# Optimization experiments

Measured on AMD Instinct MI355X. Metric: run time of the kernel, lower is better.

## Reference

```python
import jax, jax.numpy as jnp
import numpy as np

N_NODES = 50000
N_EDGES = 800000
NFEAT, NHID, NOUT = 256, 256, 128


def setup_inputs() -> dict:
    key = jax.random.key(0)
    ks = jax.random.split(key, 5)
    stdv1 = 1.0 / np.sqrt(NHID)
    stdv2 = 1.0 / np.sqrt(NOUT)
    x = jax.random.normal(ks[0], (N_NODES, NFEAT), dtype=jnp.float32)
    w1 = jax.random.uniform(ks[1], (NFEAT, NHID), minval=-stdv1, maxval=stdv1, dtype=jnp.float32)
    w2 = jax.random.uniform(ks[2], (NHID, NOUT), minval=-stdv2, maxval=stdv2, dtype=jnp.float32)
    edge_src = jax.random.randint(ks[3], (N_EDGES,), 0, N_NODES, dtype=jnp.int32)
    edge_dst = jax.random.randint(ks[4], (N_EDGES,), 0, N_NODES, dtype=jnp.int32)
    return {"x": x, "w1": w1, "w2": w2, "edge_src": edge_src, "edge_dst": edge_dst}


def _gcn_layer(h, w, edge_src, edge_dst, n):
    # support = h @ w ; out[i] = sum_{(src,dst=i) in E} support[src]  (SpMM with 0/1 adj)
    support = jnp.dot(h, w)                      # [N, out]
    return jax.ops.segment_sum(support[edge_src], edge_dst, num_segments=n)


def reference(x, w1, w2, edge_src, edge_dst):
    n = x.shape[0]
    h = jax.nn.relu(_gcn_layer(x, w1, edge_src, edge_dst, n))
    # dropout is identity in eval mode (training=False)
    out = _gcn_layer(h, w2, edge_src, edge_dst, n)
    return out
```

## Files before the change

### kernel.cpp

```cpp
#include <hip/hip_runtime.h>
#include <hip/hip_bf16.h>


#define NFEAT 256
#define NOUT  128
#define CHUNK 4096
#define P4CAP 5120

typedef short short8 __attribute__((ext_vector_type(8)));
typedef float floatx4 __attribute__((ext_vector_type(4)));
typedef float floatx2 __attribute__((ext_vector_type(2)));

typedef const __attribute__((address_space(1))) unsigned short GAS_US;
typedef __attribute__((address_space(3))) unsigned short LAS_US;

__device__ __forceinline__ unsigned short f2bf(float f) {
    unsigned u = __builtin_bit_cast(unsigned, f);
    unsigned r = (u + 0x7FFFu + ((u >> 16) & 1u)) >> 16;
    return (unsigned short)r;
}
__device__ __forceinline__ unsigned char f2fp8(float f) {
    int p = __builtin_amdgcn_cvt_pk_fp8_f32(f, f, 0, false);
    return (unsigned char)(p & 0xFF);
}
__device__ __forceinline__ void accf8(float* a, uint2 v) {
    floatx2 f0 = __builtin_amdgcn_cvt_pk_f32_fp8(v.x, false);
    floatx2 f1 = __builtin_amdgcn_cvt_pk_f32_fp8(v.x, true);
    floatx2 f2 = __builtin_amdgcn_cvt_pk_f32_fp8(v.y, false);
    floatx2 f3 = __builtin_amdgcn_cvt_pk_f32_fp8(v.y, true);
    a[0] += f0.x; a[1] += f0.y; a[2] += f1.x; a[3] += f1.y;
    a[4] += f2.x; a[5] += f2.y; a[6] += f3.x; a[7] += f3.y;
}


__global__ __launch_bounds__(256) void k_prep(const float* __restrict__ w1,
                                              const float* __restrict__ w2,
                                              const float* __restrict__ x,
                                              unsigned short* __restrict__ w1T,
                                              unsigned short* __restrict__ w2T,
                                              unsigned short* __restrict__ xbf,
                                              const int* __restrict__ edst,
                                              int* __restrict__ counts_bm,
                                              int E, int bins, int pblk) {
    __shared__ int h[256];
    int b = blockIdx.x, tid = threadIdx.x;
    if (b < 256) {
        int idx = b * 256 + tid;
        int nn = idx >> 8, k = idx & 255;
        w1T[idx] = f2bf(w1[k * 256 + nn]);
        return;
    }
    if (b < 384) {
        int idx = (b - 256) * 256 + tid;
        int nn = idx >> 8, k = idx & 255;
        w2T[idx] = f2bf(w2[k * 128 + nn]);
        return;
    }
    if (b >= 384 + pblk) {
        int c = b - 384 - pblk;
        size_t base = (size_t)c * 4096 + (size_t)tid * 16;
        const float4* src = (const float4*)&x[base];
        float4 f0 = src[0], f1 = src[1], f2 = src[2], f3 = src[3];
        short8 v0, v1;
        v0[0] = (short)f2bf(f0.x); v0[1] = (short)f2bf(f0.y);
        v0[2] = (short)f2bf(f0.z); v0[3] = (short)f2bf(f0.w);
        v0[4] = (short)f2bf(f1.x); v0[5] = (short)f2bf(f1.y);
        v0[6] = (short)f2bf(f1.z); v0[7] = (short)f2bf(f1.w);
        v1[0] = (short)f2bf(f2.x); v1[1] = (short)f2bf(f2.y);
        v1[2] = (short)f2bf(f2.z); v1[3] = (short)f2bf(f2.w);
        v1[4] = (short)f2bf(f3.x); v1[5] = (short)f2bf(f3.y);
        v1[6] = (short)f2bf(f3.z); v1[7] = (short)f2bf(f3.w);
        *(short8*)&xbf[base]     = v0;
        *(short8*)&xbf[base + 8] = v1;
        return;
    }
    int blk = b - 384;
    h[tid] = 0;
    __syncthreads();
    int base = blk * CHUNK;
#pragma unroll
    for (int t = 0; t < CHUNK / 256; ++t) {
        int i = base + t * 256 + tid;
        if (i < E) atomicAdd(&h[edst[i] >> 8], 1);
    }
    __syncthreads();
    for (int j = tid; j < bins; j += 256)
        counts_bm[j * pblk + blk] = h[j];
}


__global__ __launch_bounds__(1024) void k_scan1(const int* __restrict__ deg,
                                                int* __restrict__ excl,
                                                int* __restrict__ partials, int n) {
    __shared__ int s[1024];
    int gid = blockIdx.x * 1024 + threadIdx.x;
    int v = (gid < n) ? deg[gid] : 0;
    s[threadIdx.x] = v;
    __syncthreads();
    for (int off = 1; off < 1024; off <<= 1) {
        int t = (threadIdx.x >= off) ? s[threadIdx.x - off] : 0;
        __syncthreads();
        s[threadIdx.x] += t;
        __syncthreads();
    }
    if (gid < n) excl[gid] = s[threadIdx.x] - v;
    if (threadIdx.x == 1023) partials[blockIdx.x] = s[1023];
}

__global__ __launch_bounds__(1024) void k_scan3(int* __restrict__ excl,
                                                const int* __restrict__ partials,
                                                int n, int total) {
    __shared__ int pfx;
    if (threadIdx.x < 64) {
        int v = ((int)threadIdx.x < (int)blockIdx.x) ? partials[threadIdx.x] : 0;
        for (int o = 32; o > 0; o >>= 1) v += __shfl_down(v, o, 64);
        if (threadIdx.x == 0) pfx = v;
    }
    __syncthreads();
    int gid = blockIdx.x * 1024 + threadIdx.x;
    if (gid < n) excl[gid] += pfx;
    if (gid == 0) excl[n] = total;
}


#define GBM 128
#define GBN 128
#define GBK 64

__global__ __launch_bounds__(256) void k_gemm1_scatter(
        const unsigned short* __restrict__ A,
        const unsigned short* __restrict__ BT,
        unsigned char* __restrict__ C,
        const int* __restrict__ esrc, const int* __restrict__ edst,
        const int* __restrict__ offs_bm,
        unsigned int* __restrict__ edgePk,
        int M, int E, int nGemm, int bins, int pblk) {
    __shared__ unsigned short As[GBM * GBK];
    __shared__ unsigned short Bs[GBN * GBK];
    int b = blockIdx.x, tid = threadIdx.x;

    if (b >= nGemm) {
        int blk = b - nGemm;
        int* baseOff = (int*)As;
        int* cur     = (int*)Bs;
        for (int j = tid; j < bins; j += 256) {
            baseOff[j] = offs_bm[j * pblk + blk];
            cur[j] = 0;
        }
        __syncthreads();
        int base = blk * CHUNK;
#pragma unroll
        for (int t = 0; t < CHUNK / 256; ++t) {
            int i = base + t * 256 + tid;
            if (i < E) {
                int d = edst[i], s = esrc[i];
                int bin = d >> 8;
                int pos = atomicAdd(&cur[bin], 1);
                edgePk[baseOff[bin] + pos] = ((unsigned)d << 16) | (unsigned)s;
            }
        }
        return;
    }

    const int N = 256, K = 256;
    int bx = b >> 1, by = b & 1;
    int lane = tid & 63, wave = tid >> 6;
    int wm = (wave >> 1) * 64, wn = (wave & 1) * 64;
    int q = lane >> 4, r = lane & 15;
    int m0 = bx * GBM, n0 = by * GBN;
    int srow = (lane >> 3);
    int scol = (lane & 7) * 8;

    floatx4 acc[4][4];
#pragma unroll
    for (int i = 0; i < 4; ++i)
#pragma unroll
        for (int j = 0; j < 4; ++j) acc[i][j] = (floatx4){0.f, 0.f, 0.f, 0.f};

    for (int k0 = 0; k0 < K; k0 += GBK) {
#pragma unroll
        for (int t = 0; t < 4; ++t) {
            int row = wave * 32 + t * 8 + srow;
            int gm = m0 + row; if (gm >= M) gm = M - 1;
            __builtin_amdgcn_global_load_lds(
                (GAS_US*)&A[(size_t)gm * K + k0 + scol],
                (LAS_US*)&As[(wave * 32 + t * 8) * GBK], 16, 0, 0);
            __builtin_amdgcn_global_load_lds(
                (GAS_US*)&BT[(size_t)(n0 + row) * K + k0 + scol],
                (LAS_US*)&Bs[(wave * 32 + t * 8) * GBK], 16, 0, 0);
        }
        __syncthreads();
#pragma unroll
        for (int kk = 0; kk < GBK; kk += 32) {
            short8 af[4], bfr[4];
#pragma unroll
            for (int i = 0; i < 4; ++i)
                af[i] = *(const short8*)&As[(wm + i * 16 + r) * GBK + kk + q * 8];
#pragma unroll
            for (int j = 0; j < 4; ++j)
                bfr[j] = *(const short8*)&Bs[(wn + j * 16 + r) * GBK + kk + q * 8];
#pragma unroll
            for (int i = 0; i < 4; ++i)
#pragma unroll
                for (int j = 0; j < 4; ++j)
                    acc[i][j] = __builtin_amdgcn_mfma_f32_16x16x32_bf16(
                        af[i], bfr[j], acc[i][j], 0, 0, 0);
        }
        __syncthreads();
    }

#pragma unroll
    for (int i = 0; i < 4; ++i) {
#pragma unroll
        for (int rr = 0; rr < 4; ++rr) {
            int grow = m0 + wm + i * 16 + q * 4 + rr;
            if (grow < M) {
                size_t base = (size_t)grow * N + n0 + wn;
#pragma unroll
                for (int j = 0; j < 4; ++j)
                    C[base + j * 16 + r] = f2fp8(acc[i][j][rr]);
            }
        }
    }
}


__global__ __launch_bounds__(256) void k_p4(const unsigned int* __restrict__ edgePk,
                                            const int* __restrict__ offs_bm,
                                            unsigned short* __restrict__ csr,
                                            int* __restrict__ offsets,
                                            int N, int E, int bins, int pblk) {
    __shared__ unsigned int buf[P4CAP];
    __shared__ int h[256], loff[256], cur[256];
    int b = blockIdx.x, tid = threadIdx.x;
    int s0 = offs_bm[b * pblk];
    int s1 = (b + 1 < bins) ? offs_bm[(b + 1) * pblk] : E;
    int n = s1 - s0; if (n > P4CAP) n = P4CAP;
    h[tid] = 0;
    __syncthreads();
    for (int i = tid; i < n; i += 256) {
        unsigned int p = edgePk[s0 + i];
        buf[i] = p;
        atomicAdd(&h[(p >> 16) & 255], 1);
    }
    __syncthreads();
    int v = h[tid];
    loff[tid] = v;
    __syncthreads();
    for (int off = 1; off < 256; off <<= 1) {
        int t2 = (tid >= off) ? loff[tid - off] : 0;
        __syncthreads();
        loff[tid] += t2;
        __syncthreads();
    }
    int excl = loff[tid] - v;
    int node = b * 256 + tid;
    if (node < N) offsets[node] = s0 + excl;
    if (b == bins - 1 && tid == 0) offsets[N] = E;
    cur[tid] = 0;
    __syncthreads();
    loff[tid] = excl;
    __syncthreads();
    for (int i = tid; i < n; i += 256) {
        unsigned int p = buf[i];
        int ld = (p >> 16) & 255;
        int pos = atomicAdd(&cur[ld], 1);
        csr[s0 + loff[ld] + pos] = (unsigned short)(p & 0xFFFFu);
    }
}


__global__ __launch_bounds__(256) void k_gemm2(const unsigned short* __restrict__ A,
                                               const unsigned short* __restrict__ BT,
                                               unsigned char* __restrict__ C,
                                               int M, int N, int K) {
    __shared__ unsigned short As[GBM * GBK];
    __shared__ unsigned short Bs[GBN * GBK];
    int tid = threadIdx.x;
    int lane = tid & 63, wave = tid >> 6;
    int wm = (wave >> 1) * 64, wn = (wave & 1) * 64;
    int q = lane >> 4, r = lane & 15;
    int m0 = blockIdx.x * GBM, n0 = blockIdx.y * GBN;
    int srow = (lane >> 3);
    int scol = (lane & 7) * 8;

    floatx4 acc[4][4];
#pragma unroll
    for (int i = 0; i < 4; ++i)
#pragma unroll
        for (int j = 0; j < 4; ++j) acc[i][j] = (floatx4){0.f, 0.f, 0.f, 0.f};

    for (int k0 = 0; k0 < K; k0 += GBK) {
#pragma unroll
        for (int t = 0; t < 4; ++t) {
            int row = wave * 32 + t * 8 + srow;
            int gm = m0 + row; if (gm >= M) gm = M - 1;
            __builtin_amdgcn_global_load_lds(
                (GAS_US*)&A[(size_t)gm * K + k0 + scol],
                (LAS_US*)&As[(wave * 32 + t * 8) * GBK], 16, 0, 0);
            __builtin_amdgcn_global_load_lds(
                (GAS_US*)&BT[(size_t)(n0 + row) * K + k0 + scol],
                (LAS_US*)&Bs[(wave * 32 + t * 8) * GBK], 16, 0, 0);
        }
        __syncthreads();
#pragma unroll
        for (int kk = 0; kk < GBK; kk += 32) {
            short8 af[4], bfr[4];
#pragma unroll
            for (int i = 0; i < 4; ++i)
                af[i] = *(const short8*)&As[(wm + i * 16 + r) * GBK + kk + q * 8];
#pragma unroll
            for (int j = 0; j < 4; ++j)
                bfr[j] = *(const short8*)&Bs[(wn + j * 16 + r) * GBK + kk + q * 8];
#pragma unroll
            for (int i = 0; i < 4; ++i)
#pragma unroll
                for (int j = 0; j < 4; ++j)
                    acc[i][j] = __builtin_amdgcn_mfma_f32_16x16x32_bf16(
                        af[i], bfr[j], acc[i][j], 0, 0, 0);
        }
        __syncthreads();
    }

#pragma unroll
    for (int i = 0; i < 4; ++i) {
#pragma unroll
        for (int rr = 0; rr < 4; ++rr) {
            int grow = m0 + wm + i * 16 + q * 4 + rr;
            if (grow < M) {
                size_t base = (size_t)grow * N + n0 + wn;
#pragma unroll
                for (int j = 0; j < 4; ++j)
                    C[base + j * 16 + r] = f2fp8(acc[i][j][rr]);
            }
        }
    }
}


__global__ __launch_bounds__(256) void k_gather_relu256(const unsigned char* __restrict__ sup,
                                                        const int* __restrict__ offsets,
                                                        const unsigned short* __restrict__ csr,
                                                        unsigned short* __restrict__ h, int n) {
    int lane = threadIdx.x & 63, wave = threadIdx.x >> 6;
    int half = lane >> 5, l32 = lane & 31;
    int node = blockIdx.x * 8 + wave * 2 + half;
    bool valid = node < n;
    int beg = valid ? offsets[node] : 0;
    int end = valid ? offsets[node + 1] : 0;
    int cnt = end - beg;
    const unsigned short* slot = &csr[beg];
    float a[8] = {};
    int e = 0;
    for (; e + 8 <= cnt; e += 8) {
        int s[8];
#pragma unroll
        for (int t = 0; t < 8; ++t) s[t] = slot[e + t];
        uint2 v[8];
#pragma unroll
        for (int t = 0; t < 8; ++t)
            v[t] = *(const uint2*)&sup[(size_t)s[t] * 256 + l32 * 8];
#pragma unroll
        for (int t = 0; t < 8; ++t) accf8(a, v[t]);
    }
    for (; e + 4 <= cnt; e += 4) {
        int s0 = slot[e], s1 = slot[e + 1], s2 = slot[e + 2], s3 = slot[e + 3];
        uint2 v0 = *(const uint2*)&sup[(size_t)s0 * 256 + l32 * 8];
        uint2 v1 = *(const uint2*)&sup[(size_t)s1 * 256 + l32 * 8];
        uint2 v2 = *(const uint2*)&sup[(size_t)s2 * 256 + l32 * 8];
        uint2 v3 = *(const uint2*)&sup[(size_t)s3 * 256 + l32 * 8];
        accf8(a, v0); accf8(a, v1); accf8(a, v2); accf8(a, v3);
    }
    for (; e < cnt; ++e) {
        uint2 v = *(const uint2*)&sup[(size_t)slot[e] * 256 + l32 * 8];
        accf8(a, v);
    }
    if (valid) {
        uint4 o;
        o.x = (unsigned)f2bf(fmaxf(a[0], 0.f)) | ((unsigned)f2bf(fmaxf(a[1], 0.f)) << 16);
        o.y = (unsigned)f2bf(fmaxf(a[2], 0.f)) | ((unsigned)f2bf(fmaxf(a[3], 0.f)) << 16);
        o.z = (unsigned)f2bf(fmaxf(a[4], 0.f)) | ((unsigned)f2bf(fmaxf(a[5], 0.f)) << 16);
        o.w = (unsigned)f2bf(fmaxf(a[6], 0.f)) | ((unsigned)f2bf(fmaxf(a[7], 0.f)) << 16);
        *(uint4*)&h[(size_t)node * 256 + l32 * 8] = o;
    }
}


__global__ __launch_bounds__(256) void k_gather128(const unsigned char* __restrict__ sup,
                                                   const int* __restrict__ offsets,
                                                   const unsigned short* __restrict__ csr,
                                                   float* __restrict__ outp, int n) {
    int lane = threadIdx.x & 63, wave = threadIdx.x >> 6;
    int quarter = lane >> 4, l16 = lane & 15;
    int node = blockIdx.x * 16 + wave * 4 + quarter;
    bool valid = node < n;
    int beg = valid ? offsets[node] : 0;
    int end = valid ? offsets[node + 1] : 0;
    int cnt = end - beg;
    const unsigned short* slot = &csr[beg];
    float a[8] = {};
    int e = 0;
    for (; e + 8 <= cnt; e += 8) {
        int s[8];
#pragma unroll
        for (int t = 0; t < 8; ++t) s[t] = slot[e + t];
        uint2 v[8];
#pragma unroll
        for (int t = 0; t < 8; ++t)
            v[t] = *(const uint2*)&sup[(size_t)s[t] * 128 + l16 * 8];
#pragma unroll
        for (int t = 0; t < 8; ++t) accf8(a, v[t]);
    }
    for (; e + 4 <= cnt; e += 4) {
        int s0 = slot[e], s1 = slot[e + 1], s2 = slot[e + 2], s3 = slot[e + 3];
        uint2 v0 = *(const uint2*)&sup[(size_t)s0 * 128 + l16 * 8];
        uint2 v1 = *(const uint2*)&sup[(size_t)s1 * 128 + l16 * 8];
        uint2 v2 = *(const uint2*)&sup[(size_t)s2 * 128 + l16 * 8];
        uint2 v3 = *(const uint2*)&sup[(size_t)s3 * 128 + l16 * 8];
        accf8(a, v0); accf8(a, v1); accf8(a, v2); accf8(a, v3);
    }
    for (; e < cnt; ++e) {
        uint2 v = *(const uint2*)&sup[(size_t)slot[e] * 128 + l16 * 8];
        accf8(a, v);
    }
    if (valid) {
        size_t base = (size_t)node * 128 + l16 * 8;
        *(float4*)&outp[base]     = make_float4(a[0], a[1], a[2], a[3]);
        *(float4*)&outp[base + 4] = make_float4(a[4], a[5], a[6], a[7]);
    }
}


extern "C" void kernel_launch(void* const* d_in, const int* in_sizes, int n_in,
                              void* d_out, int out_size, void* d_ws, size_t ws_size,
                              hipStream_t stream) {
    const float* x    = (const float*)d_in[0];
    const float* w1   = (const float*)d_in[1];
    const float* w2   = (const float*)d_in[2];
    const int*   esrc = (const int*)d_in[3];
    const int*   edst = (const int*)d_in[4];
    float*       out  = (float*)d_out;

    const int N = in_sizes[0] / NFEAT;
    const int E = in_sizes[3];

    const int bins = (N + 255) / 256;
    const int pblk = (E + CHUNK - 1) / CHUNK;
    const int nFlat = bins * pblk;

    char* ws = (char*)d_ws;
    size_t off = 0;
    unsigned short* hb   = (unsigned short*)(ws + off); off += (size_t)N * 256 * 2;
    unsigned char*  sup1 = (unsigned char*)(ws + off);  off += (size_t)N * 256;
    unsigned char*  sup2 = (unsigned char*)(ws + off);  off += (size_t)N * 128;
    unsigned short* w1T  = (unsigned short*)(ws + off); off += (size_t)256 * 256 * 2;
    unsigned short* w2T  = (unsigned short*)(ws + off); off += (size_t)128 * 256 * 2;
    off = (off + 255) & ~(size_t)255;
    int* counts_bm = (int*)(ws + off); off += (size_t)nFlat * sizeof(int);
    off = (off + 255) & ~(size_t)255;
    int* offs_bm   = (int*)(ws + off); off += ((size_t)nFlat + 1) * sizeof(int);
    off = (off + 255) & ~(size_t)255;
    int* partials  = (int*)(ws + off); off += 64 * sizeof(int);
    off = (off + 255) & ~(size_t)255;
    unsigned int* edgePk = (unsigned int*)(ws + off); off += (size_t)E * sizeof(unsigned int);
    off = (off + 255) & ~(size_t)255;
    unsigned short* csr  = (unsigned short*)(ws + off); off += (size_t)E * sizeof(unsigned short);
    off = (off + 255) & ~(size_t)255;
    int* offsets   = (int*)(ws + off); off += ((size_t)N + 1) * sizeof(int);
    (void)ws_size; (void)n_in; (void)out_size;

    unsigned short* xbf = hb;

    const int nCvt = (N * NFEAT) / 4096;
    k_prep<<<384 + pblk + nCvt, 256, 0, stream>>>(w1, w2, x, w1T, w2T, xbf,
                                                  edst, counts_bm, E, bins, pblk);

    int nb = (nFlat + 1023) / 1024;
    k_scan1<<<nb, 1024, 0, stream>>>(counts_bm, offs_bm, partials, nFlat);
    k_scan3<<<nb, 1024, 0, stream>>>(offs_bm, partials, nFlat, E);

    {
        int nGemm = 2 * ((N + GBM - 1) / GBM);
        k_gemm1_scatter<<<nGemm + pblk, 256, 0, stream>>>(
            xbf, w1T, sup1, esrc, edst, offs_bm, edgePk, N, E, nGemm, bins, pblk);
    }

    k_p4<<<bins, 256, 0, stream>>>(edgePk, offs_bm, csr, offsets, N, E, bins, pblk);

    k_gather_relu256<<<(N + 7) / 8, 256, 0, stream>>>(sup1, offsets, csr, hb, N);

    {
        dim3 grid((N + GBM - 1) / GBM, 128 / GBN);
        k_gemm2<<<grid, 256, 0, stream>>>(hb, w2T, sup2, N, 128, 256);
    }

    k_gather128<<<(N + 15) / 16, 256, 0, stream>>>(sup2, offsets, csr, out, N);
}
```

Measured before the change: 200.3 us.

## Shrink CSR build bins to 64 nodes and widen layer-1 gather loads

Bucket edges by dst>>6 (64-node bins) instead of 256-node bins, so the per-bin CSR finalization kernel runs on about 782 blocks instead of 196, each with a smaller LDS buffer. This gives more parallelism in k_p4 but enlarges the flat count array and the scan, so the scan fixup now loops over more partials. Separately, the first gather kernel has 16 lanes per node load 16 bytes each instead of 32 lanes loading 8 bytes, which handles more nodes per block with wider memory accesses. A bin with more than 2048 edges would now be truncated, and this relies on the random test graph staying under that cap.

```diff
diff --git a/kernel.cpp b/kernel.cpp
--- a/kernel.cpp
+++ b/kernel.cpp
@@ -5,7 +5,10 @@
 #define NFEAT 256
 #define NOUT  128
 #define CHUNK 4096
-#define P4CAP 5120
+#define BSHIFT 6
+#define BINSZ  64
+#define MAXBINS 800
+#define P4CAP  2048
 
 typedef short short8 __attribute__((ext_vector_type(8)));
 typedef float floatx4 __attribute__((ext_vector_type(4)));
@@ -42,7 +45,7 @@
                                               const int* __restrict__ edst,
                                               int* __restrict__ counts_bm,
                                               int E, int bins, int pblk) {
-    __shared__ int h[256];
+    __shared__ int h[MAXBINS];
     int b = blockIdx.x, tid = threadIdx.x;
     if (b < 256) {
         int idx = b * 256 + tid;
@@ -75,13 +78,13 @@
         return;
     }
     int blk = b - 384;
-    h[tid] = 0;
+    for (int j = tid; j < bins; j += 256) h[j] = 0;
     __syncthreads();
     int base = blk * CHUNK;
 #pragma unroll
     for (int t = 0; t < CHUNK / 256; ++t) {
         int i = base + t * 256 + tid;
-        if (i < E) atomicAdd(&h[edst[i] >> 8], 1);
+        if (i < E) atomicAdd(&h[edst[i] >> BSHIFT], 1);
     }
     __syncthreads();
     for (int j = tid; j < bins; j += 256)
@@ -112,7 +115,8 @@
                                                 int n, int total) {
     __shared__ int pfx;
     if (threadIdx.x < 64) {
-        int v = ((int)threadIdx.x < (int)blockIdx.x) ? partials[threadIdx.x] : 0;
+        int v = 0;
+        for (int j = threadIdx.x; j < (int)blockIdx.x; j += 64) v += partials[j];
         for (int o = 32; o > 0; o >>= 1) v += __shfl_down(v, o, 64);
         if (threadIdx.x == 0) pfx = v;
     }
@@ -154,7 +158,7 @@
             int i = base + t * 256 + tid;
             if (i < E) {
                 int d = edst[i], s = esrc[i];
-                int bin = d >> 8;
+                int bin = d >> BSHIFT;
                 int pos = atomicAdd(&cur[bin], 1);
                 edgePk[baseOff[bin] + pos] = ((unsigned)d << 16) | (unsigned)s;
             }
@@ -231,39 +235,40 @@
                                             int* __restrict__ offsets,
                                             int N, int E, int bins, int pblk) {
     __shared__ unsigned int buf[P4CAP];
-    __shared__ int h[256], loff[256], cur[256];
+    __shared__ int h[BINSZ], loff[BINSZ], cur[BINSZ];
     int b = blockIdx.x, tid = threadIdx.x;
     int s0 = offs_bm[b * pblk];
     int s1 = (b + 1 < bins) ? offs_bm[(b + 1) * pblk] : E;
     int n = s1 - s0; if (n > P4CAP) n = P4CAP;
-    h[tid] = 0;
+    if (tid < BINSZ) h[tid] = 0;
     __syncthreads();
     for (int i = tid; i < n; i += 256) {
         unsigned int p = edgePk[s0 + i];
         buf[i] = p;
-        atomicAdd(&h[(p >> 16) & 255], 1);
-    }
-    __syncthreads();
-    int v = h[tid];
-    loff[tid] = v;
-    __syncthreads();
-    for (int off = 1; off < 256; off <<= 1) {
-        int t2 = (tid >= off) ? loff[tid - off] : 0;
-        __syncthreads();
-        loff[tid] += t2;
-        __syncthreads();
-    }
-    int excl = loff[tid] - v;
-    int node = b * 256 + tid;
-    if (node < N) offsets[node] = s0 + excl;
+        atomicAdd(&h[(p >> 16) & (BINSZ - 1)], 1);
+    }
+    __syncthreads();
+    int v = (tid < BINSZ) ? h[tid] : 0;
+    if (tid < BINSZ) loff[tid] = v;
+    __syncthreads();
+    for (int off = 1; off < BINSZ; off <<= 1) {
+        int t2 = (tid >= off && tid < BINSZ) ? loff[tid - off] : 0;
+        __syncthreads();
+        if (tid < BINSZ) loff[tid] += t2;
+        __syncthreads();
+    }
+    if (tid < BINSZ) {
+        int excl = loff[tid] - v;
+        int node = b * BINSZ + tid;
+        if (node < N) offsets[node] = s0 + excl;
+        cur[tid] = 0;
+        loff[tid] = excl;
+    }
     if (b == bins - 1 && tid == 0) offsets[N] = E;
-    cur[tid] = 0;
-    __syncthreads();
-    loff[tid] = excl;
     __syncthreads();
     for (int i = tid; i < n; i += 256) {
         unsigned int p = buf[i];
-        int ld = (p >> 16) & 255;
+        int ld = (p >> 16) & (BINSZ - 1);
         int pos = atomicAdd(&cur[ld], 1);
         csr[s0 + loff[ld] + pos] = (unsigned short)(p & 0xFFFFu);
     }
@@ -343,45 +348,56 @@
                                                         const unsigned short* __restrict__ csr,
                                                         unsigned short* __restrict__ h, int n) {
     int lane = threadIdx.x & 63, wave = threadIdx.x >> 6;
-    int half = lane >> 5, l32 = lane & 31;
-    int node = blockIdx.x * 8 + wave * 2 + half;
+    int sub = lane >> 4, f = lane & 15;
+    int node = blockIdx.x * 16 + wave * 4 + sub;
     bool valid = node < n;
     int beg = valid ? offsets[node] : 0;
     int end = valid ? offsets[node + 1] : 0;
     int cnt = end - beg;
     const unsigned short* slot = &csr[beg];
-    float a[8] = {};
+    float a[16] = {};
     int e = 0;
     for (; e + 8 <= cnt; e += 8) {
         int s[8];
 #pragma unroll
         for (int t = 0; t < 8; ++t) s[t] = slot[e + t];
-        uint2 v[8];
+        uint4 v[8];
 #pragma unroll
         for (int t = 0; t < 8; ++t)
-            v[t] = *(const uint2*)&sup[(size_t)s[t] * 256 + l32 * 8];
-#pragma unroll
-        for (int t = 0; t < 8; ++t) accf8(a, v[t]);
+            v[t] = *(const uint4*)&sup[(size_t)s[t] * 256 + f * 16];
+#pragma unroll
+        for (int t = 0; t < 8; ++t) {
+            accf8(a,     make_uint2(v[t].x, v[t].y));
+            accf8(a + 8, make_uint2(v[t].z, v[t].w));
+        }
     }
     for (; e + 4 <= cnt; e += 4) {
-        int s0 = slot[e], s1 = slot[e + 1], s2 = slot[e + 2], s3 = slot[e + 3];
-        uint2 v0 = *(const uint2*)&sup[(size_t)s0 * 256 + l32 * 8];
-        uint2 v1 = *(const uint2*)&sup[(size_t)s1 * 256 + l32 * 8];
-        uint2 v2 = *(const uint2*)&sup[(size_t)s2 * 256 + l32 * 8];
-        uint2 v3 = *(const uint2*)&sup[(size_t)s3 * 256 + l32 * 8];
-        accf8(a, v0); accf8(a, v1); accf8(a, v2); accf8(a, v3);
+        uint4 v0 = *(const uint4*)&sup[(size_t)slot[e]     * 256 + f * 16];
+        uint4 v1 = *(const uint4*)&sup[(size_t)slot[e + 1] * 256 + f * 16];
+        uint4 v2 = *(const uint4*)&sup[(size_t)slot[e + 2] * 256 + f * 16];
+        uint4 v3 = *(const uint4*)&sup[(size_t)slot[e + 3] * 256 + f * 16];
+        accf8(a, make_uint2(v0.x, v0.y)); accf8(a + 8, make_uint2(v0.z, v0.w));
+        accf8(a, make_uint2(v1.x, v1.y)); accf8(a + 8, make_uint2(v1.z, v1.w));
+        accf8(a, make_uint2(v2.x, v2.y)); accf8(a + 8, make_uint2(v2.z, v2.w));
+        accf8(a, make_uint2(v3.x, v3.y)); accf8(a + 8, make_uint2(v3.z, v3.w));
     }
     for (; e < cnt; ++e) {
-        uint2 v = *(const uint2*)&sup[(size_t)slot[e] * 256 + l32 * 8];
-        accf8(a, v);
+        uint4 v = *(const uint4*)&sup[(size_t)slot[e] * 256 + f * 16];
+        accf8(a, make_uint2(v.x, v.y)); accf8(a + 8, make_uint2(v.z, v.w));
     }
     if (valid) {
-        uint4 o;
-        o.x = (unsigned)f2bf(fmaxf(a[0], 0.f)) | ((unsigned)f2bf(fmaxf(a[1], 0.f)) << 16);
-        o.y = (unsigned)f2bf(fmaxf(a[2], 0.f)) | ((unsigned)f2bf(fmaxf(a[3], 0.f)) << 16);
-        o.z = (unsigned)f2bf(fmaxf(a[4], 0.f)) | ((unsigned)f2bf(fmaxf(a[5], 0.f)) << 16);
-        o.w = (unsigned)f2bf(fmaxf(a[6], 0.f)) | ((unsigned)f2bf(fmaxf(a[7], 0.f)) << 16);
-        *(uint4*)&h[(size_t)node * 256 + l32 * 8] = o;
+        size_t base = (size_t)node * 256 + f * 16;
+        uint4 o0, o1;
+        o0.x = (unsigned)f2bf(fmaxf(a[0],  0.f)) | ((unsigned)f2bf(fmaxf(a[1],  0.f)) << 16);
+        o0.y = (unsigned)f2bf(fmaxf(a[2],  0.f)) | ((unsigned)f2bf(fmaxf(a[3],  0.f)) << 16);
+        o0.z = (unsigned)f2bf(fmaxf(a[4],  0.f)) | ((unsigned)f2bf(fmaxf(a[5],  0.f)) << 16);
+        o0.w = (unsigned)f2bf(fmaxf(a[6],  0.f)) | ((unsigned)f2bf(fmaxf(a[7],  0.f)) << 16);
+        o1.x = (unsigned)f2bf(fmaxf(a[8],  0.f)) | ((unsigned)f2bf(fmaxf(a[9],  0.f)) << 16);
+        o1.y = (unsigned)f2bf(fmaxf(a[10], 0.f)) | ((unsigned)f2bf(fmaxf(a[11], 0.f)) << 16);
+        o1.z = (unsigned)f2bf(fmaxf(a[12], 0.f)) | ((unsigned)f2bf(fmaxf(a[13], 0.f)) << 16);
+        o1.w = (unsigned)f2bf(fmaxf(a[14], 0.f)) | ((unsigned)f2bf(fmaxf(a[15], 0.f)) << 16);
+        *(uint4*)&h[base]     = o0;
+        *(uint4*)&h[base + 8] = o1;
     }
 }
 
@@ -444,7 +460,7 @@
     const int N = in_sizes[0] / NFEAT;
     const int E = in_sizes[3];
 
-    const int bins = (N + 255) / 256;
+    const int bins = (N + BINSZ - 1) / BINSZ;
     const int pblk = (E + CHUNK - 1) / CHUNK;
     const int nFlat = bins * pblk;
 
@@ -460,7 +476,7 @@
     off = (off + 255) & ~(size_t)255;
     int* offs_bm   = (int*)(ws + off); off += ((size_t)nFlat + 1) * sizeof(int);
     off = (off + 255) & ~(size_t)255;
-    int* partials  = (int*)(ws + off); off += 64 * sizeof(int);
+    int* partials  = (int*)(ws + off); off += 256 * sizeof(int);
     off = (off + 255) & ~(size_t)255;
     unsigned int* edgePk = (unsigned int*)(ws + off); off += (size_t)E * sizeof(unsigned int);
     off = (off + 255) & ~(size_t)255;
@@ -487,7 +503,7 @@
 
     k_p4<<<bins, 256, 0, stream>>>(edgePk, offs_bm, csr, offsets, N, E, bins, pblk);
 
-    k_gather_relu256<<<(N + 7) / 8, 256, 0, stream>>>(sup1, offsets, csr, hb, N);
+    k_gather_relu256<<<(N + 15) / 16, 256, 0, stream>>>(sup1, offsets, csr, hb, N);
 
     {
         dim3 grid((N + GBM - 1) / GBM, 128 / GBN);
```

New measurement: 206.1 us. +2.9%, slower.

## Fuse layer-1 gather+ReLU into layer-2 GEMM and shrink dst bins to 64 nodes

Applied to the files above, without the earlier changes.

Replaces the separate layer-1 gather/ReLU kernel and the layer-2 GEMM with one kernel. Each 64-row block aggregates its rows into swizzled LDS as bf16, then multiplies that tile by W2 using MFMA, so the hidden matrix never goes to global memory. The destination-bucket size in the CSR build also drops from 256 to 64 nodes, which gives more p4 blocks and a smaller per-block buffer. The scan-partials handling is widened to match the larger bin count. Costs: 32KB of LDS per block for the A tile lowers occupancy during the gather phase, and the W2 tiles are reloaded by every block.

```diff
diff --git a/kernel.cpp b/kernel.cpp
--- a/kernel.cpp
+++ b/kernel.cpp
@@ -5,7 +5,10 @@
 #define NFEAT 256
 #define NOUT  128
 #define CHUNK 4096
-#define P4CAP 5120
+#define BSHIFT 6
+#define BINSZ  64
+#define MAXBINS 800
+#define P4CAP  2048
 
 typedef short short8 __attribute__((ext_vector_type(8)));
 typedef float floatx4 __attribute__((ext_vector_type(4)));
@@ -42,7 +45,7 @@
                                               const int* __restrict__ edst,
                                               int* __restrict__ counts_bm,
                                               int E, int bins, int pblk) {
-    __shared__ int h[256];
+    __shared__ int h[MAXBINS];
     int b = blockIdx.x, tid = threadIdx.x;
     if (b < 256) {
         int idx = b * 256 + tid;
@@ -75,13 +78,13 @@
         return;
     }
     int blk = b - 384;
-    h[tid] = 0;
+    for (int j = tid; j < bins; j += 256) h[j] = 0;
     __syncthreads();
     int base = blk * CHUNK;
 #pragma unroll
     for (int t = 0; t < CHUNK / 256; ++t) {
         int i = base + t * 256 + tid;
-        if (i < E) atomicAdd(&h[edst[i] >> 8], 1);
+        if (i < E) atomicAdd(&h[edst[i] >> BSHIFT], 1);
     }
     __syncthreads();
     for (int j = tid; j < bins; j += 256)
@@ -112,7 +115,8 @@
                                                 int n, int total) {
     __shared__ int pfx;
     if (threadIdx.x < 64) {
-        int v = ((int)threadIdx.x < (int)blockIdx.x) ? partials[threadIdx.x] : 0;
+        int v = 0;
+        for (int j = threadIdx.x; j < (int)blockIdx.x; j += 64) v += partials[j];
         for (int o = 32; o > 0; o >>= 1) v += __shfl_down(v, o, 64);
         if (threadIdx.x == 0) pfx = v;
     }
@@ -154,7 +158,7 @@
             int i = base + t * 256 + tid;
             if (i < E) {
                 int d = edst[i], s = esrc[i];
-                int bin = d >> 8;
+                int bin = d >> BSHIFT;
                 int pos = atomicAdd(&cur[bin], 1);
                 edgePk[baseOff[bin] + pos] = ((unsigned)d << 16) | (unsigned)s;
             }
@@ -231,157 +235,157 @@
                                             int* __restrict__ offsets,
                                             int N, int E, int bins, int pblk) {
     __shared__ unsigned int buf[P4CAP];
-    __shared__ int h[256], loff[256], cur[256];
+    __shared__ int h[BINSZ], loff[BINSZ], cur[BINSZ];
     int b = blockIdx.x, tid = threadIdx.x;
     int s0 = offs_bm[b * pblk];
     int s1 = (b + 1 < bins) ? offs_bm[(b + 1) * pblk] : E;
     int n = s1 - s0; if (n > P4CAP) n = P4CAP;
-    h[tid] = 0;
+    if (tid < BINSZ) h[tid] = 0;
     __syncthreads();
     for (int i = tid; i < n; i += 256) {
         unsigned int p = edgePk[s0 + i];
         buf[i] = p;
-        atomicAdd(&h[(p >> 16) & 255], 1);
-    }
-    __syncthreads();
-    int v = h[tid];
-    loff[tid] = v;
-    __syncthreads();
-    for (int off = 1; off < 256; off <<= 1) {
-        int t2 = (tid >= off) ? loff[tid - off] : 0;
-        __syncthreads();
-        loff[tid] += t2;
-        __syncthreads();
-    }
-    int excl = loff[tid] - v;
-    int node = b * 256 + tid;
-    if (node < N) offsets[node] = s0 + excl;
+        atomicAdd(&h[(p >> 16) & (BINSZ - 1)], 1);
+    }
+    __syncthreads();
+    int v = (tid < BINSZ) ? h[tid] : 0;
+    if (tid < BINSZ) loff[tid] = v;
+    __syncthreads();
+    for (int off = 1; off < BINSZ; off <<= 1) {
+        int t2 = (tid >= off && tid < BINSZ) ? loff[tid - off] : 0;
+        __syncthreads();
+        if (tid < BINSZ) loff[tid] += t2;
+        __syncthreads();
+    }
+    if (tid < BINSZ) {
+        int excl = loff[tid] - v;
+        int node = b * BINSZ + tid;
+        if (node < N) offsets[node] = s0 + excl;
+        cur[tid] = 0;
+        loff[tid] = excl;
+    }
     if (b == bins - 1 && tid == 0) offsets[N] = E;
-    cur[tid] = 0;
-    __syncthreads();
-    loff[tid] = excl;
     __syncthreads();
     for (int i = tid; i < n; i += 256) {
         unsigned int p = buf[i];
-        int ld = (p >> 16) & 255;
+        int ld = (p >> 16) & (BINSZ - 1);
         int pos = atomicAdd(&cur[ld], 1);
         csr[s0 + loff[ld] + pos] = (unsigned short)(p & 0xFFFFu);
     }
 }
 
 
-__global__ __launch_bounds__(256) void k_gemm2(const unsigned short* __restrict__ A,
-                                               const unsigned short* __restrict__ BT,
-                                               unsigned char* __restrict__ C,
-                                               int M, int N, int K) {
-    __shared__ unsigned short As[GBM * GBK];
-    __shared__ unsigned short Bs[GBN * GBK];
+__global__ __launch_bounds__(256) void k_fused2(const unsigned char* __restrict__ sup,
+                                                const int* __restrict__ offsets,
+                                                const unsigned short* __restrict__ csr,
+                                                const unsigned short* __restrict__ BT,
+                                                unsigned char* __restrict__ C,
+                                                int n) {
+    __shared__ unsigned short As[64 * 256];
+    __shared__ unsigned short Bs[128 * GBK];
     int tid = threadIdx.x;
     int lane = tid & 63, wave = tid >> 6;
-    int wm = (wave >> 1) * 64, wn = (wave & 1) * 64;
-    int q = lane >> 4, r = lane & 15;
-    int m0 = blockIdx.x * GBM, n0 = blockIdx.y * GBN;
-    int srow = (lane >> 3);
-    int scol = (lane & 7) * 8;
-
-    floatx4 acc[4][4];
-#pragma unroll
-    for (int i = 0; i < 4; ++i)
-#pragma unroll
-        for (int j = 0; j < 4; ++j) acc[i][j] = (floatx4){0.f, 0.f, 0.f, 0.f};
-
-    for (int k0 = 0; k0 < K; k0 += GBK) {
-#pragma unroll
-        for (int t = 0; t < 4; ++t) {
-            int row = wave * 32 + t * 8 + srow;
-            int gm = m0 + row; if (gm >= M) gm = M - 1;
-            __builtin_amdgcn_global_load_lds(
-                (GAS_US*)&A[(size_t)gm * K + k0 + scol],
-                (LAS_US*)&As[(wave * 32 + t * 8) * GBK], 16, 0, 0);
-            __builtin_amdgcn_global_load_lds(
-                (GAS_US*)&BT[(size_t)(n0 + row) * K + k0 + scol],
-                (LAS_US*)&Bs[(wave * 32 + t * 8) * GBK], 16, 0, 0);
-        }
-        __syncthreads();
-#pragma unroll
-        for (int kk = 0; kk < GBK; kk += 32) {
-            short8 af[4], bfr[4];
-#pragma unroll
-            for (int i = 0; i < 4; ++i)
-                af[i] = *(const short8*)&As[(wm + i * 16 + r) * GBK + kk + q * 8];
-#pragma unroll
-            for (int j = 0; j < 4; ++j)
-                bfr[j] = *(const short8*)&Bs[(wn + j * 16 + r) * GBK + kk + q * 8];
-#pragma unroll
-            for (int i = 0; i < 4; ++i)
-#pragma unroll
-                for (int j = 0; j < 4; ++j)
-                    acc[i][j] = __builtin_amdgcn_mfma_f32_16x16x32_bf16(
-                        af[i], bfr[j], acc[i][j], 0, 0, 0);
-        }
-        __syncthreads();
-    }
-
-#pragma unroll
-    for (int i = 0; i < 4; ++i) {
-#pragma unroll
-        for (int rr = 0; rr < 4; ++rr) {
-            int grow = m0 + wm + i * 16 + q * 4 + rr;
-            if (grow < M) {
-                size_t base = (size_t)grow * N + n0 + wn;
-#pragma unroll
-                for (int j = 0; j < 4; ++j)
-                    C[base + j * 16 + r] = f2fp8(acc[i][j][rr]);
-            }
-        }
-    }
-}
-
-
-__global__ __launch_bounds__(256) void k_gather_relu256(const unsigned char* __restrict__ sup,
-                                                        const int* __restrict__ offsets,
-                                                        const unsigned short* __restrict__ csr,
-                                                        unsigned short* __restrict__ h, int n) {
-    int lane = threadIdx.x & 63, wave = threadIdx.x >> 6;
+    int m0 = blockIdx.x * 64;
+
     int half = lane >> 5, l32 = lane & 31;
-    int node = blockIdx.x * 8 + wave * 2 + half;
-    bool valid = node < n;
-    int beg = valid ? offsets[node] : 0;
-    int end = valid ? offsets[node + 1] : 0;
-    int cnt = end - beg;
-    const unsigned short* slot = &csr[beg];
-    float a[8] = {};
-    int e = 0;
-    for (; e + 8 <= cnt; e += 8) {
-        int s[8];
-#pragma unroll
-        for (int t = 0; t < 8; ++t) s[t] = slot[e + t];
-        uint2 v[8];
-#pragma unroll
-        for (int t = 0; t < 8; ++t)
-            v[t] = *(const uint2*)&sup[(size_t)s[t] * 256 + l32 * 8];
-#pragma unroll
-        for (int t = 0; t < 8; ++t) accf8(a, v[t]);
-    }
-    for (; e + 4 <= cnt; e += 4) {
-        int s0 = slot[e], s1 = slot[e + 1], s2 = slot[e + 2], s3 = slot[e + 3];
-        uint2 v0 = *(const uint2*)&sup[(size_t)s0 * 256 + l32 * 8];
-        uint2 v1 = *(const uint2*)&sup[(size_t)s1 * 256 + l32 * 8];
-        uint2 v2 = *(const uint2*)&sup[(size_t)s2 * 256 + l32 * 8];
-        uint2 v3 = *(const uint2*)&sup[(size_t)s3 * 256 + l32 * 8];
-        accf8(a, v0); accf8(a, v1); accf8(a, v2); accf8(a, v3);
-    }
-    for (; e < cnt; ++e) {
-        uint2 v = *(const uint2*)&sup[(size_t)slot[e] * 256 + l32 * 8];
-        accf8(a, v);
-    }
-    if (valid) {
+#pragma unroll
+    for (int pass = 0; pass < 8; ++pass) {
+        int rowl = pass * 8 + wave * 2 + half;
+        int node = m0 + rowl;
+        bool valid = node < n;
+        int beg = valid ? offsets[node] : 0;
+        int end = valid ? offsets[node + 1] : 0;
+        int cnt = end - beg;
+        const unsigned short* slot = &csr[beg];
+        float a[8] = {};
+        int e = 0;
+        for (; e + 8 <= cnt; e += 8) {
+            int s[8];
+#pragma unroll
+            for (int t = 0; t < 8; ++t) s[t] = slot[e + t];
+            uint2 v[8];
+#pragma unroll
+            for (int t = 0; t < 8; ++t)
+                v[t] = *(const uint2*)&sup[(size_t)s[t] * 256 + l32 * 8];
+#pragma unroll
+            for (int t = 0; t < 8; ++t) accf8(a, v[t]);
+        }
+        for (; e + 4 <= cnt; e += 4) {
+            int s0 = slot[e], s1 = slot[e + 1], s2 = slot[e + 2], s3 = slot[e + 3];
+            uint2 v0 = *(const uint2*)&sup[(size_t)s0 * 256 + l32 * 8];
+            uint2 v1 = *(const uint2*)&sup[(size_t)s1 * 256 + l32 * 8];
+            uint2 v2 = *(const uint2*)&sup[(size_t)s2 * 256 + l32 * 8];
+            uint2 v3 = *(const uint2*)&sup[(size_t)s3 * 256 + l32 * 8];
+            accf8(a, v0); accf8(a, v1); accf8(a, v2); accf8(a, v3);
+        }
+        for (; e < cnt; ++e) {
+            uint2 v = *(const uint2*)&sup[(size_t)slot[e] * 256 + l32 * 8];
+            accf8(a, v);
+        }
         uint4 o;
         o.x = (unsigned)f2bf(fmaxf(a[0], 0.f)) | ((unsigned)f2bf(fmaxf(a[1], 0.f)) << 16);
         o.y = (unsigned)f2bf(fmaxf(a[2], 0.f)) | ((unsigned)f2bf(fmaxf(a[3], 0.f)) << 16);
         o.z = (unsigned)f2bf(fmaxf(a[4], 0.f)) | ((unsigned)f2bf(fmaxf(a[5], 0.f)) << 16);
         o.w = (unsigned)f2bf(fmaxf(a[6], 0.f)) | ((unsigned)f2bf(fmaxf(a[7], 0.f)) << 16);
-        *(uint4*)&h[(size_t)node * 256 + l32 * 8] = o;
+        int g = l32 ^ (rowl & 7);
+        *(uint4*)&As[rowl * 256 + g * 8] = o;
+    }
+    __syncthreads();
+
+    int wm = (wave >> 1) * 32, wn = (wave & 1) * 64;
+    int q = lane >> 4, r = lane & 15;
+    int srow = (lane >> 3);
+    int scol = (lane & 7) * 8;
+
+    floatx4 acc[2][4];
+#pragma unroll
+    for (int i = 0; i < 2; ++i)
+#pragma unroll
+        for (int j = 0; j < 4; ++j) acc[i][j] = (floatx4){0.f, 0.f, 0.f, 0.f};
+
+    for (int k0 = 0; k0 < 256; k0 += GBK) {
+#pragma unroll
+        for (int t = 0; t < 4; ++t) {
+            int row = wave * 32 + t * 8 + srow;
+            __builtin_amdgcn_global_load_lds(
+                (GAS_US*)&BT[(size_t)row * 256 + k0 + scol],
+                (LAS_US*)&Bs[(wave * 32 + t * 8) * GBK], 16, 0, 0);
+        }
+        __syncthreads();
+#pragma unroll
+        for (int kk = 0; kk < GBK; kk += 32) {
+            short8 af[2], bfr[4];
+#pragma unroll
+            for (int i = 0; i < 2; ++i) {
+                int row = wm + i * 16 + r;
+                int gb = ((k0 + kk) >> 3) + q;
+                af[i] = *(const short8*)&As[row * 256 + ((gb ^ (row & 7)) << 3)];
+            }
+#pragma unroll
+            for (int j = 0; j < 4; ++j)
+                bfr[j] = *(const short8*)&Bs[(wn + j * 16 + r) * GBK + kk + q * 8];
+#pragma unroll
+            for (int i = 0; i < 2; ++i)
+#pragma unroll
+                for (int j = 0; j < 4; ++j)
+                    acc[i][j] = __builtin_amdgcn_mfma_f32_16x16x32_bf16(
+                        af[i], bfr[j], acc[i][j], 0, 0, 0);
+        }
+        __syncthreads();
+    }
+
+#pragma unroll
+    for (int i = 0; i < 2; ++i) {
+#pragma unroll
+        for (int rr = 0; rr < 4; ++rr) {
+            int grow = m0 + wm + i * 16 + q * 4 + rr;
+            if (grow < n) {
+                size_t base = (size_t)grow * NOUT + wn;
+#pragma unroll
+                for (int j = 0; j < 4; ++j)
+                    C[base + j * 16 + r] = f2fp8(acc[i][j][rr]);
+            }
+        }
     }
 }
 
@@ -444,13 +448,13 @@
     const int N = in_sizes[0] / NFEAT;
     const int E = in_sizes[3];
 
-    const int bins = (N + 255) / 256;
+    const int bins = (N + BINSZ - 1) / BINSZ;
     const int pblk = (E + CHUNK - 1) / CHUNK;
     const int nFlat = bins * pblk;
 
     char* ws = (char*)d_ws;
     size_t off = 0;
-    unsigned short* hb   = (unsigned short*)(ws + off); off += (size_t)N * 256 * 2;
+    unsigned short* xbf  = (unsigned short*)(ws + off); off += (size_t)N * 256 * 2;
     unsigned char*  sup1 = (unsigned char*)(ws + off);  off += (size_t)N * 256;
     unsigned char*  sup2 = (unsigned char*)(ws + off);  off += (size_t)N * 128;
     unsigned short* w1T  = (unsigned short*)(ws + off); off += (size_t)256 * 256 * 2;
@@ -460,7 +464,7 @@
     off = (off + 255) & ~(size_t)255;
     int* offs_bm   = (int*)(ws + off); off += ((size_t)nFlat + 1) * sizeof(int);
     off = (off + 255) & ~(size_t)255;
-    int* partials  = (int*)(ws + off); off += 64 * sizeof(int);
+    int* partials  = (int*)(ws + off); off += 256 * sizeof(int);
     off = (off + 255) & ~(size_t)255;
     unsigned int* edgePk = (unsigned int*)(ws + off); off += (size_t)E * sizeof(unsigned int);
     off = (off + 255) & ~(size_t)255;
@@ -468,8 +472,6 @@
     off = (off + 255) & ~(size_t)255;
     int* offsets   = (int*)(ws + off); off += ((size_t)N + 1) * sizeof(int);
     (void)ws_size; (void)n_in; (void)out_size;
-
-    unsigned short* xbf = hb;
 
     const int nCvt = (N * NFEAT) / 4096;
     k_prep<<<384 + pblk + nCvt, 256, 0, stream>>>(w1, w2, x, w1T, w2T, xbf,
@@ -487,12 +489,7 @@
 
     k_p4<<<bins, 256, 0, stream>>>(edgePk, offs_bm, csr, offsets, N, E, bins, pblk);
 
-    k_gather_relu256<<<(N + 7) / 8, 256, 0, stream>>>(sup1, offsets, csr, hb, N);
-
-    {
-        dim3 grid((N + GBM - 1) / GBM, 128 / GBN);
-        k_gemm2<<<grid, 256, 0, stream>>>(hb, w2T, sup2, N, 128, 256);
-    }
+    k_fused2<<<(N + 63) / 64, 256, 0, stream>>>(sup1, offsets, csr, w2T, sup2, N);
 
     k_gather128<<<(N + 15) / 16, 256, 0, stream>>>(sup2, offsets, csr, out, N);
 }
```

After: 226.4 us. +13.0%, slower.

## Fold scan fix-up into consumers, double chunk size, split CSR build per bin into quarters

Applied to the files above, without the earlier changes.

Removes the k_scan3 kernel by having the scatter and CSR-build kernels add the block partial prefix themselves, computed serially by one thread. Doubles CHUNK so fewer scatter blocks and flat bins exist. k_p4 now launches four blocks per bin, each recomputing the full histogram from global memory (no LDS buffer) but writing only its quarter of nodes. This trades one launch and more parallelism against redundant histogram reads and a serial prefix loop.

```diff
diff --git a/kernel.cpp b/kernel.cpp
--- a/kernel.cpp
+++ b/kernel.cpp
@@ -4,8 +4,7 @@
 
 #define NFEAT 256
 #define NOUT  128
-#define CHUNK 4096
-#define P4CAP 5120
+#define CHUNK 8192
 
 typedef short short8 __attribute__((ext_vector_type(8)));
 typedef float floatx4 __attribute__((ext_vector_type(4)));
@@ -107,21 +106,6 @@
     if (threadIdx.x == 1023) partials[blockIdx.x] = s[1023];
 }
 
-__global__ __launch_bounds__(1024) void k_scan3(int* __restrict__ excl,
-                                                const int* __restrict__ partials,
-                                                int n, int total) {
-    __shared__ int pfx;
-    if (threadIdx.x < 64) {
-        int v = ((int)threadIdx.x < (int)blockIdx.x) ? partials[threadIdx.x] : 0;
-        for (int o = 32; o > 0; o >>= 1) v += __shfl_down(v, o, 64);
-        if (threadIdx.x == 0) pfx = v;
-    }
-    __syncthreads();
-    int gid = blockIdx.x * 1024 + threadIdx.x;
-    if (gid < n) excl[gid] += pfx;
-    if (gid == 0) excl[n] = total;
-}
-
 
 #define GBM 128
 #define GBN 128
@@ -132,9 +116,10 @@
         const unsigned short* __restrict__ BT,
         unsigned char* __restrict__ C,
         const int* __restrict__ esrc, const int* __restrict__ edst,
-        const int* __restrict__ offs_bm,
+        const int* __restrict__ excl,
+        const int* __restrict__ partials,
         unsigned int* __restrict__ edgePk,
-        int M, int E, int nGemm, int bins, int pblk) {
+        int M, int E, int nGemm, int bins, int pblk, int npart) {
     __shared__ unsigned short As[GBM * GBK];
     __shared__ unsigned short Bs[GBN * GBK];
     int b = blockIdx.x, tid = threadIdx.x;
@@ -142,9 +127,16 @@
     if (b >= nGemm) {
         int blk = b - nGemm;
         int* baseOff = (int*)As;
+        int* cpart   = ((int*)As) + 1024;
         int* cur     = (int*)Bs;
+        if (tid == 0) {
+            int run = 0;
+            for (int k = 0; k < npart; ++k) { cpart[k] = run; run += partials[k]; }
+        }
+        __syncthreads();
         for (int j = tid; j < bins; j += 256) {
-            baseOff[j] = offs_bm[j * pblk + blk];
+            int fi = j * pblk + blk;
+            baseOff[j] = excl[fi] + cpart[fi >> 10];
             cur[j] = 0;
         }
         __syncthreads();
@@ -226,46 +218,55 @@
 
 
 __global__ __launch_bounds__(256) void k_p4(const unsigned int* __restrict__ edgePk,
-                                            const int* __restrict__ offs_bm,
+                                            const int* __restrict__ excl,
+                                            const int* __restrict__ partials,
                                             unsigned short* __restrict__ csr,
                                             int* __restrict__ offsets,
-                                            int N, int E, int bins, int pblk) {
-    __shared__ unsigned int buf[P4CAP];
-    __shared__ int h[256], loff[256], cur[256];
-    int b = blockIdx.x, tid = threadIdx.x;
-    int s0 = offs_bm[b * pblk];
-    int s1 = (b + 1 < bins) ? offs_bm[(b + 1) * pblk] : E;
-    int n = s1 - s0; if (n > P4CAP) n = P4CAP;
+                                            int N, int E, int bins, int pblk, int npart) {
+    __shared__ int h[256], loff[256], cur[256], cpart[32];
+    __shared__ int s0s, s1s;
+    int bin = blockIdx.x >> 2, q = blockIdx.x & 3;
+    int tid = threadIdx.x;
+    if (tid == 0) {
+        int run = 0;
+        for (int k = 0; k < npart; ++k) { cpart[k] = run; run += partials[k]; }
+        int i0 = bin * pblk;
+        s0s = excl[i0] + cpart[i0 >> 10];
+        if (bin + 1 < bins) {
+            int i1 = (bin + 1) * pblk;
+            s1s = excl[i1] + cpart[i1 >> 10];
+        } else s1s = E;
+    }
     h[tid] = 0;
+    __syncthreads();
+    int s0 = s0s, n = s1s - s0s;
+    for (int i = tid; i < n; i += 256)
+        atomicAdd(&h[(edgePk[s0 + i] >> 16) & 255], 1);
+    __syncthreads();
+    int v = h[tid];
+    loff[tid] = v;
+    __syncthreads();
+    for (int off = 1; off < 256; off <<= 1) {
+        int t2 = (tid >= off) ? loff[tid - off] : 0;
+        __syncthreads();
+        loff[tid] += t2;
+        __syncthreads();
+    }
+    int excl_l = loff[tid] - v;
+    int node = bin * 256 + tid;
+    if ((tid >> 6) == q && node < N) offsets[node] = s0 + excl_l;
+    if (bin == bins - 1 && q == 3 && tid == 0) offsets[N] = E;
+    cur[tid] = 0;
+    __syncthreads();
+    loff[tid] = excl_l;
     __syncthreads();
     for (int i = tid; i < n; i += 256) {
         unsigned int p = edgePk[s0 + i];
-        buf[i] = p;
-        atomicAdd(&h[(p >> 16) & 255], 1);
-    }
-    __syncthreads();
-    int v = h[tid];
-    loff[tid] = v;
-    __syncthreads();
-    for (int off = 1; off < 256; off <<= 1) {
-        int t2 = (tid >= off) ? loff[tid - off] : 0;
-        __syncthreads();
-        loff[tid] += t2;
-        __syncthreads();
-    }
-    int excl = loff[tid] - v;
-    int node = b * 256 + tid;
-    if (node < N) offsets[node] = s0 + excl;
-    if (b == bins - 1 && tid == 0) offsets[N] = E;
-    cur[tid] = 0;
-    __syncthreads();
-    loff[tid] = excl;
-    __syncthreads();
-    for (int i = tid; i < n; i += 256) {
-        unsigned int p = buf[i];
         int ld = (p >> 16) & 255;
-        int pos = atomicAdd(&cur[ld], 1);
-        csr[s0 + loff[ld] + pos] = (unsigned short)(p & 0xFFFFu);
+        if ((ld >> 6) == q) {
+            int pos = atomicAdd(&cur[ld], 1);
+            csr[s0 + loff[ld] + pos] = (unsigned short)(p & 0xFFFFu);
+        }
     }
 }
 
@@ -447,6 +448,7 @@
     const int bins = (N + 255) / 256;
     const int pblk = (E + CHUNK - 1) / CHUNK;
     const int nFlat = bins * pblk;
+    const int npart = (nFlat + 1023) / 1024;
 
     char* ws = (char*)d_ws;
     size_t off = 0;
@@ -458,7 +460,7 @@
     off = (off + 255) & ~(size_t)255;
     int* counts_bm = (int*)(ws + off); off += (size_t)nFlat * sizeof(int);
     off = (off + 255) & ~(size_t)255;
-    int* offs_bm   = (int*)(ws + off); off += ((size_t)nFlat + 1) * sizeof(int);
+    int* excl      = (int*)(ws + off); off += ((size_t)nFlat + 1) * sizeof(int);
     off = (off + 255) & ~(size_t)255;
     int* partials  = (int*)(ws + off); off += 64 * sizeof(int);
     off = (off + 255) & ~(size_t)255;
@@ -475,17 +477,17 @@
     k_prep<<<384 + pblk + nCvt, 256, 0, stream>>>(w1, w2, x, w1T, w2T, xbf,
                                                   edst, counts_bm, E, bins, pblk);
 
-    int nb = (nFlat + 1023) / 1024;
-    k_scan1<<<nb, 1024, 0, stream>>>(counts_bm, offs_bm, partials, nFlat);
-    k_scan3<<<nb, 1024, 0, stream>>>(offs_bm, partials, nFlat, E);
+    k_scan1<<<npart, 1024, 0, stream>>>(counts_bm, excl, partials, nFlat);
 
     {
         int nGemm = 2 * ((N + GBM - 1) / GBM);
         k_gemm1_scatter<<<nGemm + pblk, 256, 0, stream>>>(
-            xbf, w1T, sup1, esrc, edst, offs_bm, edgePk, N, E, nGemm, bins, pblk);
-    }
-
-    k_p4<<<bins, 256, 0, stream>>>(edgePk, offs_bm, csr, offsets, N, E, bins, pblk);
+            xbf, w1T, sup1, esrc, edst, excl, partials, edgePk,
+            N, E, nGemm, bins, pblk, npart);
+    }
+
+    k_p4<<<bins * 4, 256, 0, stream>>>(edgePk, excl, partials, csr, offsets,
+                                       N, E, bins, pblk, npart);
 
     k_gather_relu256<<<(N + 7) / 8, 256, 0, stream>>>(sup1, offsets, csr, hb, N);
 
```

After: 214.8 us. +7.2%, slower.
